# Optimization experiments

Hardware: AMD Instinct MI355X
Metric: run time of the kernel (lower is better)

The kernel has to match this reference:

```python
import jax, jax.numpy as jnp
import numpy as np

EPSILON = 0.01            # params.epsilon (cluster precision regularizer)
GAMMA = 0.005             # params.gamma (outlier/uniform component weight)
FIX_CLUSTER_POS_ITER = 1  # params.fix_cluster_pos_iter


def _sqdist(TVs, X):
    # TVs: (M, 3, N) transformed points, X: (K, 3) cluster means -> (M, N, K)
    return ((TVs ** 2).sum(1)[:, :, None]
            + (X ** 2).sum(1)[None, None, :]
            - 2.0 * jnp.einsum('mdn,kd->mnk', TVs, X))


def setup_inputs() -> dict:
    key = jax.random.key(0)
    kV, kX, kQ = jax.random.split(key, 3)
    M, N, K = 8, 8192, 256
    Vs = jax.random.normal(kV, (M, 3, N), dtype=jnp.float32)      # 3D point clouds
    X0 = jax.random.normal(kX, (K, 3), dtype=jnp.float32)         # init cluster means (sphere init)
    Q0 = 0.1 + 0.2 * jax.random.uniform(kQ, (K,), dtype=jnp.float32)  # init cluster precisions
    return {"Vs": Vs, "X0": X0, "Q0": Q0, "num_iters": 6}


def reference(Vs, X0, Q0, num_iters):
    M, _, N = Vs.shape
    K = X0.shape[0]
    dtype = Vs.dtype

    # mean_init: init_R = I, init_t = -mean(V) per view
    t0 = -Vs.mean(axis=2, keepdims=True)          # (M, 3, 1)
    TVs = Vs + t0
    beta = GAMMA * jnp.mean(Q0) ** 1.5            # get_default_beta(Q, gamma)

    X, Q = X0, Q0
    ds = _sqdist(TVs, X)                          # (M, N, K)
    R = jnp.broadcast_to(jnp.eye(3, dtype=dtype), (M, 3, 3))
    t = t0[:, :, 0]

    for i in range(num_iters):
        if i != num_iters - 1:  # detach everything except backprop_iter = [last]
            X = jax.lax.stop_gradient(X)
            Q = jax.lax.stop_gradient(Q)
            ds = jax.lax.stop_gradient(ds)

        # E-step: soft posteriors with uniform outlier component beta
        ap = jnp.exp(-0.5 * ds * Q) * Q ** 1.5    # (M, N, K); priors = 1, pyz_feature = 1
        a = ap / (ap.sum(axis=-1, keepdims=True) + beta)

        # M-step: weighted sufficient statistics
        L = a.sum(axis=1)                                   # (M, K)
        W = jnp.einsum('mdn,mnk->mdk', Vs, a) * Q           # (M, 3, K)
        mW = W.sum(axis=-1)                                 # (M, 3)
        b = L * Q                                           # (M, K)
        mX = jnp.einsum('mk,kd->md', b, X)                  # (M, 3)
        z = b.sum(axis=-1)                                  # (M,)

        # P = (W @ X)^T - mX mW^T / z  : 3x3 weighted cross-covariance per view
        P = (jnp.einsum('mdk,ke->med', W, X)
             - mX[:, :, None] * mW[:, None, :] / z[:, None, None])

        # batched Procrustes: R = U diag(1,1,det(U V^T)) V^T
        U, _, Vt = jnp.linalg.svd(P)
        det = jnp.linalg.det(jnp.einsum('mij,mjk->mik', U, Vt))
        sgn = jnp.concatenate([jnp.ones((M, 2), dtype), det[:, None]], axis=1)
        R = jnp.einsum('mij,mjk->mik', U * sgn[:, None, :], Vt)   # (M, 3, 3)
        t = (mX - jnp.einsum('mij,mj->mi', R, mW)) / z[:, None]   # (M, 3)
        TVs = jnp.einsum('mij,mjn->min', R, Vs) + t[:, :, None]   # (M, 3, N)

        # shared cluster updates (sum over views)
        den = L.sum(axis=0)                                 # (K,)
        if i > FIX_CLUSTER_POS_ITER:
            X = jnp.einsum('mdn,mnk->kd', TVs, a) / den[:, None]
        ds = _sqdist(TVs, X)
        wn = (a * ds).sum(axis=(0, 1))                      # (K,)
        Q = 3.0 * den / (wn + 3.0 * den * EPSILON)

    return TVs, R, t, X
```

## Files before the change

### kernel.cpp

```cpp
#include <hip/hip_runtime.h>
#include <math.h>

#define Mv 8
#define Nv 8192
#define Kv 256
#define BPM 64
#define NBLK (Mv*BPM)
#define NPB (Nv/BPM)
#define NITER 6
#define EPSILON_C 0.01f
#define GAMMA_C 0.005f

#define SWZK(k) ((((k)&63)<<2)|((k)>>6))
#define SWZP(p) ((((p)&31)<<2)|((p)>>5))

#define WS_R     0
#define WS_T     72
#define WS_X     96
#define WS_Q     864
#define WS_BETA  1120
#define WS_ACC   1124
#define AC_STATS 0
#define AC_L     128
#define AC_W     2176
#define AC_H     8320
#define ACCSZ    10368

__device__ __forceinline__ float wave_red_sum(float x) {
  int v;
  float t;
  v = __builtin_bit_cast(int, x);
  t = __builtin_bit_cast(float, __builtin_amdgcn_update_dpp(0, v, 0x111, 0xf, 0xf, true));
  x += t; v = __builtin_bit_cast(int, x);
  t = __builtin_bit_cast(float, __builtin_amdgcn_update_dpp(0, v, 0x112, 0xf, 0xf, true));
  x += t; v = __builtin_bit_cast(int, x);
  t = __builtin_bit_cast(float, __builtin_amdgcn_update_dpp(0, v, 0x114, 0xf, 0xf, true));
  x += t; v = __builtin_bit_cast(int, x);
  t = __builtin_bit_cast(float, __builtin_amdgcn_update_dpp(0, v, 0x118, 0xf, 0xf, true));
  x += t; v = __builtin_bit_cast(int, x);
  t = __builtin_bit_cast(float, __builtin_amdgcn_update_dpp(0, v, 0x142, 0xa, 0xf, false));
  x += t; v = __builtin_bit_cast(int, x);
  t = __builtin_bit_cast(float, __builtin_amdgcn_update_dpp(0, v, 0x143, 0xc, 0xf, false));
  x += t;
  return __builtin_bit_cast(float, __builtin_amdgcn_readlane(__builtin_bit_cast(int, x), 63));
}

__device__ __forceinline__ float quad_red_sum(float x) {
  int v = __builtin_bit_cast(int, x);
  float t = __builtin_bit_cast(float, __builtin_amdgcn_update_dpp(0, v, 0xB1, 0xf, 0xf, true));
  x += t; v = __builtin_bit_cast(int, x);
  t = __builtin_bit_cast(float, __builtin_amdgcn_update_dpp(0, v, 0x4E, 0xf, 0xf, true));
  x += t;
  return x;
}

__device__ __forceinline__ float sel4(int c, float a0, float a1, float a2, float a3) {
  float r = a0;
  r = (c==1) ? a1 : r;
  r = (c==2) ? a2 : r;
  r = (c==3) ? a3 : r;
  return r;
}

__global__ __launch_bounds__(256) void p0_init(const float* __restrict__ Vs,
                                               const float* __restrict__ X0,
                                               const float* __restrict__ Q0,
                                               float* __restrict__ ws) {
  __shared__ float sred[4];
  int tid = threadIdx.x;
  int b = blockIdx.x;
  int wave = tid >> 6, lane = tid & 63;
  if (b < 24) {
    int m = b / 3, d = b % 3;
    const float* src = Vs + (size_t)(m*3 + d) * Nv;
    float s = 0.f;
    for (int n = tid; n < Nv; n += 256) s += src[n];
    s = wave_red_sum(s);
    if (lane == 0) sred[wave] = s;
    __syncthreads();
    if (tid == 0) {
      float tot = sred[0]+sred[1]+sred[2]+sred[3];
      ws[WS_T + m*3 + d] = -tot / (float)Nv;
    }
    if (d == 0 && tid < 9) {
      ws[WS_R + m*9 + tid] = (tid==0||tid==4||tid==8) ? 1.f : 0.f;
    }
  } else {
    float s = (tid < Kv) ? Q0[tid] : 0.f;
    s = wave_red_sum(s);
    if (lane == 0) sred[wave] = s;
    __syncthreads();
    if (tid == 0) {
      float mq = (sred[0]+sred[1]+sred[2]+sred[3]) / (float)Kv;
      ws[WS_BETA] = GAMMA_C * mq * sqrtf(mq);
    }
    if (tid < Kv) ws[WS_Q + tid] = Q0[tid];
    for (int i = tid; i < Kv*3; i += 256) ws[WS_X + i] = X0[i];
    for (int i = tid; i < ACCSZ; i += 256) ws[WS_ACC + i] = 0.f;
  }
}

#define JROTF(app,aqq,apq,apr,aqr, vp0,vp1,vp2, vq0,vq1,vq2) do {           \
    float tau_ = (aqq - app) * __builtin_amdgcn_rcpf(2.0f*apq);             \
    float tt_ = __builtin_amdgcn_rcpf(fabsf(tau_) +                         \
                   __builtin_amdgcn_sqrtf(fmaf(tau_,tau_,1.0f)));           \
    tt_ = (tau_ < 0.0f) ? -tt_ : tt_;                                       \
    tt_ = (apq == 0.0f) ? 0.0f : tt_;                                       \
    float c_ = __builtin_amdgcn_rsqf(fmaf(tt_,tt_,1.0f)), s_ = tt_*c_;      \
    float papq_ = apq;                                                      \
    app = fmaf(-tt_,papq_,app); aqq = fmaf(tt_,papq_,aqq); apq = 0.0f;      \
    float tp_ = apr, tq_ = aqr;                                             \
    apr = c_*tp_ - s_*tq_; aqr = s_*tp_ + c_*tq_;                           \
    tp_=vp0; tq_=vq0; vp0=c_*tp_-s_*tq_; vq0=s_*tp_+c_*tq_;                 \
    tp_=vp1; tq_=vq1; vp1=c_*tp_-s_*tq_; vq1=s_*tp_+c_*tq_;                 \
    tp_=vp2; tq_=vq2; vp2=c_*tp_-s_*tq_; vq2=s_*tp_+c_*tq_;                 \
  } while(0)

#define CSWAP3F(la,lb, a0,a1,a2, b0,b1,b2) do {                             \
    if (la < lb) { float t_;                                                \
      t_=la; la=lb; lb=t_; t_=a0; a0=b0; b0=t_;                             \
      t_=a1; a1=b1; b1=t_; t_=a2; a2=b2; b2=t_; }                           \
  } while(0)

template<int ITPREV>
__device__ __forceinline__ void small_update(const float* __restrict__ acc,
                                             const float* __restrict__ ws,
                                             int tid,
                                             float (*sX)[3], float* sQ,
                                             float (*sR)[9], float (*sT)[3],
                                             float* sTn) {
  const int k = tid;
  float lk[Mv], w0v[Mv], w1v[Mv], w2v[Mv], hk[Mv];
  #pragma unroll
  for (int mm=0;mm<Mv;mm++) {
    lk[mm]  = acc[AC_L + mm*Kv + k];
    w0v[mm] = acc[AC_W + (mm*3+0)*Kv + k];
    w1v[mm] = acc[AC_W + (mm*3+1)*Kv + k];
    w2v[mm] = acc[AC_W + (mm*3+2)*Kv + k];
    hk[mm]  = acc[AC_H + mm*Kv + k];
  }
  float xp0 = 0.f, xp1 = 0.f, xp2 = 0.f;
  if (ITPREV <= 1) {
    xp0 = ws[WS_X + k*3+0]; xp1 = ws[WS_X + k*3+1]; xp2 = ws[WS_X + k*3+2];
  }

  if (tid < Mv) {
    int mm = tid;
    const float* st = acc + AC_STATS + mm*16;
    float s0=st[0], s1=st[1], s2v=st[2], s3=st[3], s4=st[4], s5=st[5],
          s6=st[6], s7=st[7], s8=st[8], s9=st[9], s10=st[10], s11=st[11],
          s12=st[12], s13=st[13], s14=st[14], s15=st[15];
    float z = s0;
    float mX0 = s1, mX1 = s2v, mX2 = s3;
    float mW0 = s4, mW1 = s5, mW2 = s6;
    float iz = __builtin_amdgcn_rcpf(z);
    float P00 = s7  - mX0*mW0*iz;
    float P01 = s8  - mX0*mW1*iz;
    float P02 = s9  - mX0*mW2*iz;
    float P10 = s10 - mX1*mW0*iz;
    float P11 = s11 - mX1*mW1*iz;
    float P12 = s12 - mX1*mW2*iz;
    float P20 = s13 - mX2*mW0*iz;
    float P21 = s14 - mX2*mW1*iz;
    float P22 = s15 - mX2*mW2*iz;
    float a00 = P00*P00 + P10*P10 + P20*P20;
    float a01 = P00*P01 + P10*P11 + P20*P21;
    float a02 = P00*P02 + P10*P12 + P20*P22;
    float a11 = P01*P01 + P11*P11 + P21*P21;
    float a12 = P01*P02 + P11*P12 + P21*P22;
    float a22 = P02*P02 + P12*P12 + P22*P22;
    float v00=1, v01=0, v02=0, v10=0, v11=1, v12=0, v20=0, v21=0, v22=1;
    #pragma unroll 1
    for (int sweep = 0; sweep < 8; sweep++) {
      JROTF(a00,a11,a01, a02,a12, v00,v10,v20, v01,v11,v21);
      JROTF(a00,a22,a02, a01,a12, v00,v10,v20, v02,v12,v22);
      JROTF(a11,a22,a12, a01,a02, v01,v11,v21, v02,v12,v22);
    }
    float l0 = a00, l1 = a11, l2 = a22;
    CSWAP3F(l0,l1, v00,v10,v20, v01,v11,v21);
    CSWAP3F(l1,l2, v01,v11,v21, v02,v12,v22);
    CSWAP3F(l0,l1, v00,v10,v20, v01,v11,v21);
    float detP = P00*(P11*P22-P12*P21) - P01*(P10*P22-P12*P20)
               + P02*(P10*P21-P11*P20);
    float s2d = (detP < 0.0f) ? -1.0f : 1.0f;
    float tiny = 1e-18f*l0 + 1e-30f;
    float w0i = __builtin_amdgcn_rsqf(fmaxf(l0,tiny));
    float w1i = __builtin_amdgcn_rsqf(fmaxf(l1,tiny));
    float w2i = s2d*__builtin_amdgcn_rsqf(fmaxf(l2,tiny));
    float M00 = w0i*v00*v00 + w1i*v01*v01 + w2i*v02*v02;
    float M01 = w0i*v00*v10 + w1i*v01*v11 + w2i*v02*v12;
    float M02 = w0i*v00*v20 + w1i*v01*v21 + w2i*v02*v22;
    float M11 = w0i*v10*v10 + w1i*v11*v11 + w2i*v12*v12;
    float M12 = w0i*v10*v20 + w1i*v11*v21 + w2i*v12*v22;
    float M22 = w0i*v20*v20 + w1i*v21*v21 + w2i*v22*v22;
    float R00n = P00*M00 + P01*M01 + P02*M02;
    float R01n = P00*M01 + P01*M11 + P02*M12;
    float R02n = P00*M02 + P01*M12 + P02*M22;
    float R10n = P10*M00 + P11*M01 + P12*M02;
    float R11n = P10*M01 + P11*M11 + P12*M12;
    float R12n = P10*M02 + P11*M12 + P12*M22;
    float R20n = P20*M00 + P21*M01 + P22*M02;
    float R21n = P20*M01 + P21*M11 + P22*M12;
    float R22n = P20*M02 + P21*M12 + P22*M22;
    float tm0 = (mX0 - (R00n*mW0 + R01n*mW1 + R02n*mW2))*iz;
    float tm1 = (mX1 - (R10n*mW0 + R11n*mW1 + R12n*mW2))*iz;
    float tm2 = (mX2 - (R20n*mW0 + R21n*mW1 + R22n*mW2))*iz;
    sR[mm][0]=R00n; sR[mm][1]=R01n; sR[mm][2]=R02n;
    sR[mm][3]=R10n; sR[mm][4]=R11n; sR[mm][5]=R12n;
    sR[mm][6]=R20n; sR[mm][7]=R21n; sR[mm][8]=R22n;
    sT[mm][0]=tm0; sT[mm][1]=tm1; sT[mm][2]=tm2;
    sTn[mm] = tm0*tm0 + tm1*tm1 + tm2*tm2;
  }
  __syncthreads();
  {
    float den = 0.f, Xn0=0.f, Xn1=0.f, Xn2=0.f, S2=0.f;
    #pragma unroll
    for (int mm=0;mm<Mv;mm++) {
      float r0 = sR[mm][0]*w0v[mm] + sR[mm][1]*w1v[mm] + sR[mm][2]*w2v[mm];
      float r1 = sR[mm][3]*w0v[mm] + sR[mm][4]*w1v[mm] + sR[mm][5]*w2v[mm];
      float r2 = sR[mm][6]*w0v[mm] + sR[mm][7]*w1v[mm] + sR[mm][8]*w2v[mm];
      float tt0 = sT[mm][0], tt1 = sT[mm][1], tt2 = sT[mm][2];
      den += lk[mm];
      Xn0 += r0 + tt0*lk[mm]; Xn1 += r1 + tt1*lk[mm]; Xn2 += r2 + tt2*lk[mm];
      S2  += hk[mm] + 2.f*(tt0*r0+tt1*r1+tt2*r2) + sTn[mm]*lk[mm];
    }
    float x0, x1, x2;
    if (ITPREV > 1) { float inv = __builtin_amdgcn_rcpf(den);
                      x0=Xn0*inv; x1=Xn1*inv; x2=Xn2*inv; }
    else            { x0=xp0; x1=xp1; x2=xp2; }
    float wn = S2 + (x0*x0+x1*x1+x2*x2)*den - 2.f*(x0*Xn0+x1*Xn1+x2*Xn2);
    float qn = 3.f*den / (wn + 3.f*den*EPSILON_C);
    sX[k][0]=x0; sX[k][1]=x1; sX[k][2]=x2;
    sQ[k] = qn;
  }
}

template<int IT>
__global__ __launch_bounds__(256) void p_iter(const float* __restrict__ Vs,
                                              float* __restrict__ ws) {
  __shared__ __align__(16) float sC4[Kv][4];
  __shared__ float sKC[Kv];
  __shared__ __align__(16) float sP4[NPB][4];
  __shared__ __align__(16) float sV4[NPB][4];
  __shared__ float sLi[NPB];
  __shared__ float st4[4][16];
  __shared__ float sX[Kv][3];
  __shared__ float sQ[Kv];
  __shared__ float sR[Mv][9];
  __shared__ float sT[Mv][3];
  __shared__ float sTn[Mv];

  int tid  = threadIdx.x;
  int wave = tid >> 6, lane = tid & 63;
  int bid  = blockIdx.x;
  int m    = bid / BPM;
  int blk  = bid % BPM;
  int n0   = blk * NPB;

  float* acc  = ws + WS_ACC + (IT % 3)*ACCSZ;
  float* accz = ws + WS_ACC + ((IT+1) % 3)*ACCSZ;
  float beta = ws[WS_BETA];

  if (IT == 0) {
    if (tid < 72) ((float*)sR)[tid] = ws[WS_R + tid];
    if (tid < 24) ((float*)sT)[tid] = ws[WS_T + tid];
    sX[tid][0] = ws[WS_X + 3*tid+0];
    sX[tid][1] = ws[WS_X + 3*tid+1];
    sX[tid][2] = ws[WS_X + 3*tid+2];
    sQ[tid]    = ws[WS_Q + tid];
  } else {
    const float* accp = ws + WS_ACC + ((IT+2) % 3)*ACCSZ;
    small_update<(IT > 0) ? (IT-1) : 0>(accp, ws, tid, sX, sQ, sR, sT, sTn);
  }
  __syncthreads();

  { int base = bid*21;
    if (tid < 21 && base + tid < ACCSZ) accz[base + tid] = 0.f; }

  const float L2E = 1.4426950408889634f;
  {
    float xx = sX[tid][0], xy = sX[tid][1], xz = sX[tid][2];
    float q  = sQ[tid];
    float qL = q * L2E;
    float kA = -0.5f*qL;
    float kB = kA*(xx*xx+xy*xy+xz*xz);
    float kQ32 = q*sqrtf(q);
    int rr = SWZK(tid);
    *reinterpret_cast<float4*>(&sC4[rr][0]) = make_float4(qL*xx, qL*xy, qL*xz, kA);
    sKC[rr] = kQ32 * __builtin_amdgcn_exp2f(kB);
  }
  if (tid < NPB) {
    float R00=sR[m][0],R01=sR[m][1],R02=sR[m][2];
    float R10=sR[m][3],R11=sR[m][4],R12=sR[m][5];
    float R20=sR[m][6],R21=sR[m][7],R22=sR[m][8];
    float t0=sT[m][0], t1=sT[m][1], t2=sT[m][2];
    int n = n0 + tid;
    float vx = Vs[(size_t)(m*3+0)*Nv + n];
    float vy = Vs[(size_t)(m*3+1)*Nv + n];
    float vz = Vs[(size_t)(m*3+2)*Nv + n];
    float px = fmaf(R00,vx, fmaf(R01,vy, fmaf(R02,vz, t0)));
    float py = fmaf(R10,vx, fmaf(R11,vy, fmaf(R12,vz, t1)));
    float pz = fmaf(R20,vx, fmaf(R21,vy, fmaf(R22,vz, t2)));
    float tvn = fmaf(px,px, fmaf(py,py, pz*pz));
    float vn  = fmaf(vx,vx, fmaf(vy,vy, vz*vz));
    int pr = SWZP(tid);
    *reinterpret_cast<float4*>(&sP4[pr][0]) = make_float4(px,py,pz,tvn);
    *reinterpret_cast<float4*>(&sV4[pr][0]) = make_float4(vx,vy,vz,vn);
  }
  __syncthreads();

  {
    int ks = tid & 3, pg = tid >> 2;
    float4 P0 = *reinterpret_cast<const float4*>(&sP4[SWZP(2*pg+0)][0]);
    float4 P1 = *reinterpret_cast<const float4*>(&sP4[SWZP(2*pg+1)][0]);
    float s0 = 0.f, s1 = 0.f;
    #pragma unroll 4
    for (int j = 0; j < Kv/4; j++) {
      int row = (j<<2) | ks;
      float4 c4 = *reinterpret_cast<const float4*>(&sC4[row][0]);
      float kc = sKC[row];
      float a0 = fmaf(P0.x,c4.x, fmaf(P0.y,c4.y, fmaf(P0.z,c4.z, P0.w*c4.w)));
      float a1 = fmaf(P1.x,c4.x, fmaf(P1.y,c4.y, fmaf(P1.z,c4.z, P1.w*c4.w)));
      s0 = fmaf(__builtin_amdgcn_exp2f(a0), kc, s0);
      s1 = fmaf(__builtin_amdgcn_exp2f(a1), kc, s1);
    }
    float S0 = quad_red_sum(s0);
    float S1 = quad_red_sum(s1);
    if (ks < 2) {
      float Ssel = (ks == 1) ? S1 : S0;
      sLi[SWZP(2*pg + ks)] = -__log2f(Ssel + beta);
    }
  }
  __syncthreads();

  float cXx0,cXy0,cXz0,cA0,cC0, cXx1,cXy1,cXz1,cA1,cC1,
        cXx2,cXy2,cXz2,cA2,cC2, cXx3,cXy3,cXz3,cA3,cC3;
  {
    int kg = tid >> 2;
    #define LDC(c) { int rr = SWZK(4*kg + c); \
      float4 t4 = *reinterpret_cast<const float4*>(&sC4[rr][0]); \
      cXx##c=t4.x; cXy##c=t4.y; cXz##c=t4.z; cA##c=t4.w; cC##c=sKC[rr]; }
    LDC(0) LDC(1) LDC(2) LDC(3)
    #undef LDC
  }
  float L0=0,L1=0,L2=0,L3=0, Wx0=0,Wx1=0,Wx2=0,Wx3=0,
        Wy0=0,Wy1=0,Wy2=0,Wy3=0, Wz0=0,Wz1=0,Wz2=0,Wz3=0,
        H0=0,H1=0,H2=0,H3=0;
  {
    int ns = tid & 3;
    #pragma unroll 4
    for (int j = 0; j < NPB/4; j++) {
      int prow = (j<<2) | ns;
      float4 p4 = *reinterpret_cast<const float4*>(&sP4[prow][0]);
      float4 v4 = *reinterpret_cast<const float4*>(&sV4[prow][0]);
      float li = sLi[prow];
      #define P2K(c) { \
        float arg = fmaf(p4.w, cA##c, li); \
        arg = fmaf(p4.x, cXx##c, fmaf(p4.y, cXy##c, fmaf(p4.z, cXz##c, arg))); \
        float e = __builtin_amdgcn_exp2f(arg) * cC##c; \
        L##c += e; \
        Wx##c = fmaf(e, v4.x, Wx##c); Wy##c = fmaf(e, v4.y, Wy##c); \
        Wz##c = fmaf(e, v4.z, Wz##c); H##c  = fmaf(e, v4.w, H##c); }
      P2K(0) P2K(1) P2K(2) P2K(3)
      #undef P2K
    }
  }
  L0=quad_red_sum(L0); L1=quad_red_sum(L1); L2=quad_red_sum(L2); L3=quad_red_sum(L3);
  Wx0=quad_red_sum(Wx0); Wx1=quad_red_sum(Wx1); Wx2=quad_red_sum(Wx2); Wx3=quad_red_sum(Wx3);
  Wy0=quad_red_sum(Wy0); Wy1=quad_red_sum(Wy1); Wy2=quad_red_sum(Wy2); Wy3=quad_red_sum(Wy3);
  Wz0=quad_red_sum(Wz0); Wz1=quad_red_sum(Wz1); Wz2=quad_red_sum(Wz2); Wz3=quad_red_sum(Wz3);
  H0=quad_red_sum(H0); H1=quad_red_sum(H1); H2=quad_red_sum(H2); H3=quad_red_sum(H3);
  int c = tid & 3;
  float vL  = sel4(c, L0,L1,L2,L3);
  float vWx = sel4(c, Wx0,Wx1,Wx2,Wx3);
  float vWy = sel4(c, Wy0,Wy1,Wy2,Wy3);
  float vWz = sel4(c, Wz0,Wz1,Wz2,Wz3);
  float vH  = sel4(c, H0,H1,H2,H3);
  atomicAdd(&acc[AC_L + m*Kv + tid], vL);
  atomicAdd(&acc[AC_W + (m*3+0)*Kv + tid], vWx);
  atomicAdd(&acc[AC_W + (m*3+1)*Kv + tid], vWy);
  atomicAdd(&acc[AC_W + (m*3+2)*Kv + tid], vWz);
  atomicAdd(&acc[AC_H + m*Kv + tid], vH);

  {
    float q  = sQ[tid];
    float x0 = sX[tid][0], x1 = sX[tid][1], x2 = sX[tid][2];
    float bk = vL*q;
    float sw0 = vWx*q, sw1 = vWy*q, sw2 = vWz*q;
    float pr[16];
    pr[0]=bk;  pr[1]=bk*x0; pr[2]=bk*x1; pr[3]=bk*x2;
    pr[4]=sw0; pr[5]=sw1;   pr[6]=sw2;
    pr[7]=sw0*x0;  pr[8]=sw1*x0;  pr[9]=sw2*x0;
    pr[10]=sw0*x1; pr[11]=sw1*x1; pr[12]=sw2*x1;
    pr[13]=sw0*x2; pr[14]=sw1*x2; pr[15]=sw2*x2;
    float red[16];
    #pragma unroll
    for (int v2=0; v2<16; v2++) red[v2] = wave_red_sum(pr[v2]);
    if (lane == 0) {
      #pragma unroll
      for (int v2=0; v2<16; v2++) st4[wave][v2] = red[v2];
    }
    __syncthreads();
    if (tid < 16)
      atomicAdd(&acc[AC_STATS + m*16 + ((tid + blk) & 15)],
                st4[0][(tid+blk)&15]+st4[1][(tid+blk)&15]+
                st4[2][(tid+blk)&15]+st4[3][(tid+blk)&15]);
  }
}

#define OUT_TOTAL (Mv*3*Nv + 72 + 24 + Kv*3)
__global__ __launch_bounds__(256) void p3_final(const float* __restrict__ Vs,
                                                const float* __restrict__ ws,
                                                float* __restrict__ out) {
  __shared__ float sX[Kv][3];
  __shared__ float sQ[Kv];
  __shared__ float sR[Mv][9];
  __shared__ float sT[Mv][3];
  __shared__ float sTn[Mv];
  int tid = threadIdx.x;
  const float* acc = ws + WS_ACC + ((NITER-1) % 3)*ACCSZ;
  small_update<NITER-1>(acc, ws, tid, sX, sQ, sR, sT, sTn);
  __syncthreads();

  for (int idx = blockIdx.x*256 + tid; idx < OUT_TOTAL; idx += 256*256) {
    if (idx < Mv*3*Nv) {
      int m = idx / (3*Nv);
      int r = idx % (3*Nv);
      int d = r / Nv;
      int n = r % Nv;
      float vx = Vs[(size_t)(m*3+0)*Nv + n];
      float vy = Vs[(size_t)(m*3+1)*Nv + n];
      float vz = Vs[(size_t)(m*3+2)*Nv + n];
      out[idx] = fmaf(sR[m][d*3+0],vx,
                 fmaf(sR[m][d*3+1],vy,
                 fmaf(sR[m][d*3+2],vz, sT[m][d])));
    } else {
      int j = idx - Mv*3*Nv;
      float v;
      if (j < 72)      v = ((float*)sR)[j];
      else if (j < 96) v = ((float*)sT)[j-72];
      else             v = ((float*)sX)[j-96];
      out[idx] = v;
    }
  }
}

extern "C" void kernel_launch(void* const* d_in, const int* in_sizes, int n_in,
                              void* d_out, int out_size, void* d_ws, size_t ws_size,
                              hipStream_t stream) {
  const float* Vs = (const float*)d_in[0];
  const float* X0 = (const float*)d_in[1];
  const float* Q0 = (const float*)d_in[2];
  float* out = (float*)d_out;
  float* ws  = (float*)d_ws;

  p0_init<<<25, 256, 0, stream>>>(Vs, X0, Q0, ws);
  p_iter<0><<<NBLK, 256, 0, stream>>>(Vs, ws);
  p_iter<1><<<NBLK, 256, 0, stream>>>(Vs, ws);
  p_iter<2><<<NBLK, 256, 0, stream>>>(Vs, ws);
  p_iter<3><<<NBLK, 256, 0, stream>>>(Vs, ws);
  p_iter<4><<<NBLK, 256, 0, stream>>>(Vs, ws);
  p_iter<5><<<NBLK, 256, 0, stream>>>(Vs, ws);
  p3_final<<<256, 256, 0, stream>>>(Vs, ws, out);
}
```

Measured before the change: 183.6 us.

## Fuse all iterations into one persistent kernel with grid-wide barriers

Replaces the init kernel, six per-iteration launches and the final kernel with a single persistent kernel that loops over iterations and uses an atomic counter barrier between them. Each block keeps its slice of points in shared memory across iterations and computes the view mean and beta itself, which removes launch gaps and repeated global reloads of Vs. Final outputs are written from shared data per block. It relies on all 512 blocks being co-resident, or the barrier deadlocks. The memset only zeroes the barrier and the first accumulator buffer, so correctness depends on the in-kernel zeroing of the other rotating buffers.

```diff
diff --git a/kernel.cpp b/kernel.cpp
--- a/kernel.cpp
+++ b/kernel.cpp
@@ -6,6 +6,7 @@
 #define Kv 256
 #define BPM 64
 #define NBLK (Mv*BPM)
+#define NBLK_U 512u
 #define NPB (Nv/BPM)
 #define NITER 6
 #define EPSILON_C 0.01f
@@ -14,17 +15,26 @@
 #define SWZK(k) ((((k)&63)<<2)|((k)>>6))
 #define SWZP(p) ((((p)&31)<<2)|((p)>>5))
 
-#define WS_R     0
-#define WS_T     72
-#define WS_X     96
-#define WS_Q     864
-#define WS_BETA  1120
-#define WS_ACC   1124
+#define WS_BAR   0
+#define WS_ACC   16
 #define AC_STATS 0
 #define AC_L     128
 #define AC_W     2176
 #define AC_H     8320
 #define ACCSZ    10368
+
+__device__ __forceinline__ void gsync(unsigned* bar, int tid) {
+  __threadfence();
+  __syncthreads();
+  if (tid == 0) {
+    __hip_atomic_fetch_add(bar, 1u, __ATOMIC_RELEASE, __HIP_MEMORY_SCOPE_AGENT);
+    while (__hip_atomic_load(bar, __ATOMIC_ACQUIRE, __HIP_MEMORY_SCOPE_AGENT) < NBLK_U) {
+      __builtin_amdgcn_s_sleep(2);
+    }
+  }
+  __syncthreads();
+  __threadfence();
+}
 
 __device__ __forceinline__ float wave_red_sum(float x) {
   int v;
@@ -60,44 +70,6 @@
   r = (c==2) ? a2 : r;
   r = (c==3) ? a3 : r;
   return r;
-}
-
-__global__ __launch_bounds__(256) void p0_init(const float* __restrict__ Vs,
-                                               const float* __restrict__ X0,
-                                               const float* __restrict__ Q0,
-                                               float* __restrict__ ws) {
-  __shared__ float sred[4];
-  int tid = threadIdx.x;
-  int b = blockIdx.x;
-  int wave = tid >> 6, lane = tid & 63;
-  if (b < 24) {
-    int m = b / 3, d = b % 3;
-    const float* src = Vs + (size_t)(m*3 + d) * Nv;
-    float s = 0.f;
-    for (int n = tid; n < Nv; n += 256) s += src[n];
-    s = wave_red_sum(s);
-    if (lane == 0) sred[wave] = s;
-    __syncthreads();
-    if (tid == 0) {
-      float tot = sred[0]+sred[1]+sred[2]+sred[3];
-      ws[WS_T + m*3 + d] = -tot / (float)Nv;
-    }
-    if (d == 0 && tid < 9) {
-      ws[WS_R + m*9 + tid] = (tid==0||tid==4||tid==8) ? 1.f : 0.f;
-    }
-  } else {
-    float s = (tid < Kv) ? Q0[tid] : 0.f;
-    s = wave_red_sum(s);
-    if (lane == 0) sred[wave] = s;
-    __syncthreads();
-    if (tid == 0) {
-      float mq = (sred[0]+sred[1]+sred[2]+sred[3]) / (float)Kv;
-      ws[WS_BETA] = GAMMA_C * mq * sqrtf(mq);
-    }
-    if (tid < Kv) ws[WS_Q + tid] = Q0[tid];
-    for (int i = tid; i < Kv*3; i += 256) ws[WS_X + i] = X0[i];
-    for (int i = tid; i < ACCSZ; i += 256) ws[WS_ACC + i] = 0.f;
-  }
 }
 
 #define JROTF(app,aqq,apq,apr,aqr, vp0,vp1,vp2, vq0,vq1,vq2) do {           \
@@ -122,13 +94,12 @@
       t_=a1; a1=b1; b1=t_; t_=a2; a2=b2; b2=t_; }                           \
   } while(0)
 
-template<int ITPREV>
-__device__ __forceinline__ void small_update(const float* __restrict__ acc,
-                                             const float* __restrict__ ws,
-                                             int tid,
-                                             float (*sX)[3], float* sQ,
-                                             float (*sR)[9], float (*sT)[3],
-                                             float* sTn) {
+__device__ __forceinline__ void small_update_rt(const float* __restrict__ acc,
+                                                const float* __restrict__ X0,
+                                                bool useX0, int tid,
+                                                float (*sX)[3], float* sQ,
+                                                float (*sR)[9], float (*sT)[3],
+                                                float* sTn) {
   const int k = tid;
   float lk[Mv], w0v[Mv], w1v[Mv], w2v[Mv], hk[Mv];
   #pragma unroll
@@ -140,8 +111,8 @@
     hk[mm]  = acc[AC_H + mm*Kv + k];
   }
   float xp0 = 0.f, xp1 = 0.f, xp2 = 0.f;
-  if (ITPREV <= 1) {
-    xp0 = ws[WS_X + k*3+0]; xp1 = ws[WS_X + k*3+1]; xp2 = ws[WS_X + k*3+2];
+  if (useX0) {
+    xp0 = X0[k*3+0]; xp1 = X0[k*3+1]; xp2 = X0[k*3+2];
   }
 
   if (tid < Mv) {
@@ -225,9 +196,9 @@
       S2  += hk[mm] + 2.f*(tt0*r0+tt1*r1+tt2*r2) + sTn[mm]*lk[mm];
     }
     float x0, x1, x2;
-    if (ITPREV > 1) { float inv = __builtin_amdgcn_rcpf(den);
-                      x0=Xn0*inv; x1=Xn1*inv; x2=Xn2*inv; }
-    else            { x0=xp0; x1=xp1; x2=xp2; }
+    if (!useX0) { float inv = __builtin_amdgcn_rcpf(den);
+                  x0=Xn0*inv; x1=Xn1*inv; x2=Xn2*inv; }
+    else        { x0=xp0; x1=xp1; x2=xp2; }
     float wn = S2 + (x0*x0+x1*x1+x2*x2)*den - 2.f*(x0*Xn0+x1*Xn1+x2*Xn2);
     float qn = 3.f*den / (wn + 3.f*den*EPSILON_C);
     sX[k][0]=x0; sX[k][1]=x1; sX[k][2]=x2;
@@ -235,9 +206,12 @@
   }
 }
 
-template<int IT>
-__global__ __launch_bounds__(256) void p_iter(const float* __restrict__ Vs,
-                                              float* __restrict__ ws) {
+#define OUT_TVS (Mv*3*Nv)
+__global__ __launch_bounds__(256, 2) void fused(const float* __restrict__ Vs,
+                                                const float* __restrict__ X0,
+                                                const float* __restrict__ Q0,
+                                                float* __restrict__ ws,
+                                                float* __restrict__ out) {
   __shared__ __align__(16) float sC4[Kv][4];
   __shared__ float sKC[Kv];
   __shared__ __align__(16) float sP4[NPB][4];
@@ -249,6 +223,8 @@
   __shared__ float sR[Mv][9];
   __shared__ float sT[Mv][3];
   __shared__ float sTn[Mv];
+  __shared__ float sredq[4];
+  __shared__ float sredt[12];
 
   int tid  = threadIdx.x;
   int wave = tid >> 6, lane = tid & 63;
@@ -257,190 +233,208 @@
   int blk  = bid % BPM;
   int n0   = blk * NPB;
 
-  float* acc  = ws + WS_ACC + (IT % 3)*ACCSZ;
-  float* accz = ws + WS_ACC + ((IT+1) % 3)*ACCSZ;
-  float beta = ws[WS_BETA];
-
-  if (IT == 0) {
-    if (tid < 72) ((float*)sR)[tid] = ws[WS_R + tid];
-    if (tid < 24) ((float*)sT)[tid] = ws[WS_T + tid];
-    sX[tid][0] = ws[WS_X + 3*tid+0];
-    sX[tid][1] = ws[WS_X + 3*tid+1];
-    sX[tid][2] = ws[WS_X + 3*tid+2];
-    sQ[tid]    = ws[WS_Q + tid];
-  } else {
-    const float* accp = ws + WS_ACC + ((IT+2) % 3)*ACCSZ;
-    small_update<(IT > 0) ? (IT-1) : 0>(accp, ws, tid, sX, sQ, sR, sT, sTn);
-  }
+  unsigned* bar = reinterpret_cast<unsigned*>(ws) + WS_BAR;
+  float* accs = ws + WS_ACC;
+
+  float q_own = Q0[tid];
+  { float s = wave_red_sum(q_own);
+    if (lane == 0) sredq[wave] = s; }
+
+  const float* V0 = Vs + (size_t)(m*3+0)*Nv;
+  const float* V1 = Vs + (size_t)(m*3+1)*Nv;
+  const float* V2 = Vs + (size_t)(m*3+2)*Nv;
+  { float sx=0.f, sy=0.f, sz=0.f;
+    for (int n = tid; n < Nv; n += 256) { sx += V0[n]; sy += V1[n]; sz += V2[n]; }
+    sx = wave_red_sum(sx); sy = wave_red_sum(sy); sz = wave_red_sum(sz);
+    if (lane == 0) { sredt[wave] = sx; sredt[4+wave] = sy; sredt[8+wave] = sz; } }
   __syncthreads();
-
-  { int base = bid*21;
-    if (tid < 21 && base + tid < ACCSZ) accz[base + tid] = 0.f; }
+  float beta;
+  { float mq = (sredq[0]+sredq[1]+sredq[2]+sredq[3]) * (1.f/(float)Kv);
+    beta = GAMMA_C * mq * sqrtf(mq); }
+  float t00 = -(sredt[0]+sredt[1]+sredt[2]+sredt[3]) * (1.f/(float)Nv);
+  float t01 = -(sredt[4]+sredt[5]+sredt[6]+sredt[7]) * (1.f/(float)Nv);
+  float t02 = -(sredt[8]+sredt[9]+sredt[10]+sredt[11]) * (1.f/(float)Nv);
+
+  float vx=0.f, vy=0.f, vz=0.f, vn=0.f;
+  if (tid < NPB) {
+    int n = n0 + tid;
+    vx = V0[n]; vy = V1[n]; vz = V2[n];
+    vn = fmaf(vx,vx, fmaf(vy,vy, vz*vz));
+    *reinterpret_cast<float4*>(&sV4[SWZP(tid)][0]) = make_float4(vx,vy,vz,vn);
+  }
 
   const float L2E = 1.4426950408889634f;
-  {
-    float xx = sX[tid][0], xy = sX[tid][1], xz = sX[tid][2];
-    float q  = sQ[tid];
-    float qL = q * L2E;
-    float kA = -0.5f*qL;
-    float kB = kA*(xx*xx+xy*xy+xz*xz);
-    float kQ32 = q*sqrtf(q);
-    int rr = SWZK(tid);
-    *reinterpret_cast<float4*>(&sC4[rr][0]) = make_float4(qL*xx, qL*xy, qL*xz, kA);
-    sKC[rr] = kQ32 * __builtin_amdgcn_exp2f(kB);
-  }
-  if (tid < NPB) {
-    float R00=sR[m][0],R01=sR[m][1],R02=sR[m][2];
-    float R10=sR[m][3],R11=sR[m][4],R12=sR[m][5];
-    float R20=sR[m][6],R21=sR[m][7],R22=sR[m][8];
-    float t0=sT[m][0], t1=sT[m][1], t2=sT[m][2];
-    int n = n0 + tid;
-    float vx = Vs[(size_t)(m*3+0)*Nv + n];
-    float vy = Vs[(size_t)(m*3+1)*Nv + n];
-    float vz = Vs[(size_t)(m*3+2)*Nv + n];
-    float px = fmaf(R00,vx, fmaf(R01,vy, fmaf(R02,vz, t0)));
-    float py = fmaf(R10,vx, fmaf(R11,vy, fmaf(R12,vz, t1)));
-    float pz = fmaf(R20,vx, fmaf(R21,vy, fmaf(R22,vz, t2)));
-    float tvn = fmaf(px,px, fmaf(py,py, pz*pz));
-    float vn  = fmaf(vx,vx, fmaf(vy,vy, vz*vz));
-    int pr = SWZP(tid);
-    *reinterpret_cast<float4*>(&sP4[pr][0]) = make_float4(px,py,pz,tvn);
-    *reinterpret_cast<float4*>(&sV4[pr][0]) = make_float4(vx,vy,vz,vn);
-  }
+  #pragma unroll 1
+  for (int it = 0; it < NITER; ++it) {
+    float* acc  = accs + (it % 3)*ACCSZ;
+    float* accz = accs + ((it+1) % 3)*ACCSZ;
+
+    if (it == 0) {
+      sX[tid][0] = X0[3*tid+0];
+      sX[tid][1] = X0[3*tid+1];
+      sX[tid][2] = X0[3*tid+2];
+      sQ[tid]    = q_own;
+    } else {
+      const float* accp = accs + ((it+2) % 3)*ACCSZ;
+      small_update_rt(accp, X0, (it-1) <= 1, tid, sX, sQ, sR, sT, sTn);
+    }
+    __syncthreads();
+
+    if (it < NITER-1) {
+      int base = bid*21;
+      if (tid < 21 && base + tid < ACCSZ) accz[base + tid] = 0.f;
+    }
+
+    float R00,R01,R02,R10,R11,R12,R20,R21,R22, t0,t1,t2;
+    if (it == 0) {
+      R00=1;R01=0;R02=0; R10=0;R11=1;R12=0; R20=0;R21=0;R22=1;
+      t0=t00; t1=t01; t2=t02;
+    } else {
+      R00=sR[m][0];R01=sR[m][1];R02=sR[m][2];
+      R10=sR[m][3];R11=sR[m][4];R12=sR[m][5];
+      R20=sR[m][6];R21=sR[m][7];R22=sR[m][8];
+      t0=sT[m][0]; t1=sT[m][1]; t2=sT[m][2];
+    }
+
+    {
+      float xx = sX[tid][0], xy = sX[tid][1], xz = sX[tid][2];
+      float q  = sQ[tid];
+      float qL = q * L2E;
+      float kA = -0.5f*qL;
+      float kB = kA*(xx*xx+xy*xy+xz*xz);
+      float kQ32 = q*sqrtf(q);
+      int rr = SWZK(tid);
+      *reinterpret_cast<float4*>(&sC4[rr][0]) = make_float4(qL*xx, qL*xy, qL*xz, kA);
+      sKC[rr] = kQ32 * __builtin_amdgcn_exp2f(kB);
+    }
+    if (tid < NPB) {
+      float px = fmaf(R00,vx, fmaf(R01,vy, fmaf(R02,vz, t0)));
+      float py = fmaf(R10,vx, fmaf(R11,vy, fmaf(R12,vz, t1)));
+      float pz = fmaf(R20,vx, fmaf(R21,vy, fmaf(R22,vz, t2)));
+      float tvn = fmaf(px,px, fmaf(py,py, pz*pz));
+      *reinterpret_cast<float4*>(&sP4[SWZP(tid)][0]) = make_float4(px,py,pz,tvn);
+    }
+    __syncthreads();
+
+    {
+      int ks = tid & 3, pg = tid >> 2;
+      float4 P0 = *reinterpret_cast<const float4*>(&sP4[SWZP(2*pg+0)][0]);
+      float4 P1 = *reinterpret_cast<const float4*>(&sP4[SWZP(2*pg+1)][0]);
+      float s0 = 0.f, s1 = 0.f;
+      #pragma unroll 4
+      for (int j = 0; j < Kv/4; j++) {
+        int row = (j<<2) | ks;
+        float4 c4 = *reinterpret_cast<const float4*>(&sC4[row][0]);
+        float kc = sKC[row];
+        float a0 = fmaf(P0.x,c4.x, fmaf(P0.y,c4.y, fmaf(P0.z,c4.z, P0.w*c4.w)));
+        float a1 = fmaf(P1.x,c4.x, fmaf(P1.y,c4.y, fmaf(P1.z,c4.z, P1.w*c4.w)));
+        s0 = fmaf(__builtin_amdgcn_exp2f(a0), kc, s0);
+        s1 = fmaf(__builtin_amdgcn_exp2f(a1), kc, s1);
+      }
+      float S0 = quad_red_sum(s0);
+      float S1 = quad_red_sum(s1);
+      if (ks < 2) {
+        float Ssel = (ks == 1) ? S1 : S0;
+        sLi[SWZP(2*pg + ks)] = -__log2f(Ssel + beta);
+      }
+    }
+    __syncthreads();
+
+    float cXx0,cXy0,cXz0,cA0,cC0, cXx1,cXy1,cXz1,cA1,cC1,
+          cXx2,cXy2,cXz2,cA2,cC2, cXx3,cXy3,cXz3,cA3,cC3;
+    {
+      int kg = tid >> 2;
+      #define LDC(c) { int rr = SWZK(4*kg + c); \
+        float4 t4 = *reinterpret_cast<const float4*>(&sC4[rr][0]); \
+        cXx##c=t4.x; cXy##c=t4.y; cXz##c=t4.z; cA##c=t4.w; cC##c=sKC[rr]; }
+      LDC(0) LDC(1) LDC(2) LDC(3)
+      #undef LDC
+    }
+    float L0=0,L1=0,L2=0,L3=0, Wx0=0,Wx1=0,Wx2=0,Wx3=0,
+          Wy0=0,Wy1=0,Wy2=0,Wy3=0, Wz0=0,Wz1=0,Wz2=0,Wz3=0,
+          H0=0,H1=0,H2=0,H3=0;
+    {
+      int ns = tid & 3;
+      #pragma unroll 4
+      for (int j = 0; j < NPB/4; j++) {
+        int prow = (j<<2) | ns;
+        float4 p4 = *reinterpret_cast<const float4*>(&sP4[prow][0]);
+        float4 v4 = *reinterpret_cast<const float4*>(&sV4[prow][0]);
+        float li = sLi[prow];
+        #define P2K(c) { \
+          float arg = fmaf(p4.w, cA##c, li); \
+          arg = fmaf(p4.x, cXx##c, fmaf(p4.y, cXy##c, fmaf(p4.z, cXz##c, arg))); \
+          float e = __builtin_amdgcn_exp2f(arg) * cC##c; \
+          L##c += e; \
+          Wx##c = fmaf(e, v4.x, Wx##c); Wy##c = fmaf(e, v4.y, Wy##c); \
+          Wz##c = fmaf(e, v4.z, Wz##c); H##c  = fmaf(e, v4.w, H##c); }
+        P2K(0) P2K(1) P2K(2) P2K(3)
+        #undef P2K
+      }
+    }
+    L0=quad_red_sum(L0); L1=quad_red_sum(L1); L2=quad_red_sum(L2); L3=quad_red_sum(L3);
+    Wx0=quad_red_sum(Wx0); Wx1=quad_red_sum(Wx1); Wx2=quad_red_sum(Wx2); Wx3=quad_red_sum(Wx3);
+    Wy0=quad_red_sum(Wy0); Wy1=quad_red_sum(Wy1); Wy2=quad_red_sum(Wy2); Wy3=quad_red_sum(Wy3);
+    Wz0=quad_red_sum(Wz0); Wz1=quad_red_sum(Wz1); Wz2=quad_red_sum(Wz2); Wz3=quad_red_sum(Wz3);
+    H0=quad_red_sum(H0); H1=quad_red_sum(H1); H2=quad_red_sum(H2); H3=quad_red_sum(H3);
+    int c = tid & 3;
+    float vL  = sel4(c, L0,L1,L2,L3);
+    float vWx = sel4(c, Wx0,Wx1,Wx2,Wx3);
+    float vWy = sel4(c, Wy0,Wy1,Wy2,Wy3);
+    float vWz = sel4(c, Wz0,Wz1,Wz2,Wz3);
+    float vH  = sel4(c, H0,H1,H2,H3);
+    atomicAdd(&acc[AC_L + m*Kv + tid], vL);
+    atomicAdd(&acc[AC_W + (m*3+0)*Kv + tid], vWx);
+    atomicAdd(&acc[AC_W + (m*3+1)*Kv + tid], vWy);
+    atomicAdd(&acc[AC_W + (m*3+2)*Kv + tid], vWz);
+    atomicAdd(&acc[AC_H + m*Kv + tid], vH);
+
+    {
+      float q  = sQ[tid];
+      float x0 = sX[tid][0], x1 = sX[tid][1], x2 = sX[tid][2];
+      float bk = vL*q;
+      float sw0 = vWx*q, sw1 = vWy*q, sw2 = vWz*q;
+      float pr[16];
+      pr[0]=bk;  pr[1]=bk*x0; pr[2]=bk*x1; pr[3]=bk*x2;
+      pr[4]=sw0; pr[5]=sw1;   pr[6]=sw2;
+      pr[7]=sw0*x0;  pr[8]=sw1*x0;  pr[9]=sw2*x0;
+      pr[10]=sw0*x1; pr[11]=sw1*x1; pr[12]=sw2*x1;
+      pr[13]=sw0*x2; pr[14]=sw1*x2; pr[15]=sw2*x2;
+      float red[16];
+      #pragma unroll
+      for (int v2=0; v2<16; v2++) red[v2] = wave_red_sum(pr[v2]);
+      if (lane == 0) {
+        #pragma unroll
+        for (int v2=0; v2<16; v2++) st4[wave][v2] = red[v2];
+      }
+      __syncthreads();
+      if (tid < 16)
+        atomicAdd(&acc[AC_STATS + m*16 + ((tid + blk) & 15)],
+                  st4[0][(tid+blk)&15]+st4[1][(tid+blk)&15]+
+                  st4[2][(tid+blk)&15]+st4[3][(tid+blk)&15]);
+    }
+
+    gsync(bar + it, tid);
+  }
+
+  small_update_rt(accs + ((NITER-1) % 3)*ACCSZ, X0, false, tid, sX, sQ, sR, sT, sTn);
   __syncthreads();
 
-  {
-    int ks = tid & 3, pg = tid >> 2;
-    float4 P0 = *reinterpret_cast<const float4*>(&sP4[SWZP(2*pg+0)][0]);
-    float4 P1 = *reinterpret_cast<const float4*>(&sP4[SWZP(2*pg+1)][0]);
-    float s0 = 0.f, s1 = 0.f;
-    #pragma unroll 4
-    for (int j = 0; j < Kv/4; j++) {
-      int row = (j<<2) | ks;
-      float4 c4 = *reinterpret_cast<const float4*>(&sC4[row][0]);
-      float kc = sKC[row];
-      float a0 = fmaf(P0.x,c4.x, fmaf(P0.y,c4.y, fmaf(P0.z,c4.z, P0.w*c4.w)));
-      float a1 = fmaf(P1.x,c4.x, fmaf(P1.y,c4.y, fmaf(P1.z,c4.z, P1.w*c4.w)));
-      s0 = fmaf(__builtin_amdgcn_exp2f(a0), kc, s0);
-      s1 = fmaf(__builtin_amdgcn_exp2f(a1), kc, s1);
-    }
-    float S0 = quad_red_sum(s0);
-    float S1 = quad_red_sum(s1);
-    if (ks < 2) {
-      float Ssel = (ks == 1) ? S1 : S0;
-      sLi[SWZP(2*pg + ks)] = -__log2f(Ssel + beta);
-    }
-  }
-  __syncthreads();
-
-  float cXx0,cXy0,cXz0,cA0,cC0, cXx1,cXy1,cXz1,cA1,cC1,
-        cXx2,cXy2,cXz2,cA2,cC2, cXx3,cXy3,cXz3,cA3,cC3;
-  {
-    int kg = tid >> 2;
-    #define LDC(c) { int rr = SWZK(4*kg + c); \
-      float4 t4 = *reinterpret_cast<const float4*>(&sC4[rr][0]); \
-      cXx##c=t4.x; cXy##c=t4.y; cXz##c=t4.z; cA##c=t4.w; cC##c=sKC[rr]; }
-    LDC(0) LDC(1) LDC(2) LDC(3)
-    #undef LDC
-  }
-  float L0=0,L1=0,L2=0,L3=0, Wx0=0,Wx1=0,Wx2=0,Wx3=0,
-        Wy0=0,Wy1=0,Wy2=0,Wy3=0, Wz0=0,Wz1=0,Wz2=0,Wz3=0,
-        H0=0,H1=0,H2=0,H3=0;
-  {
-    int ns = tid & 3;
-    #pragma unroll 4
-    for (int j = 0; j < NPB/4; j++) {
-      int prow = (j<<2) | ns;
-      float4 p4 = *reinterpret_cast<const float4*>(&sP4[prow][0]);
-      float4 v4 = *reinterpret_cast<const float4*>(&sV4[prow][0]);
-      float li = sLi[prow];
-      #define P2K(c) { \
-        float arg = fmaf(p4.w, cA##c, li); \
-        arg = fmaf(p4.x, cXx##c, fmaf(p4.y, cXy##c, fmaf(p4.z, cXz##c, arg))); \
-        float e = __builtin_amdgcn_exp2f(arg) * cC##c; \
-        L##c += e; \
-        Wx##c = fmaf(e, v4.x, Wx##c); Wy##c = fmaf(e, v4.y, Wy##c); \
-        Wz##c = fmaf(e, v4.z, Wz##c); H##c  = fmaf(e, v4.w, H##c); }
-      P2K(0) P2K(1) P2K(2) P2K(3)
-      #undef P2K
-    }
-  }
-  L0=quad_red_sum(L0); L1=quad_red_sum(L1); L2=quad_red_sum(L2); L3=quad_red_sum(L3);
-  Wx0=quad_red_sum(Wx0); Wx1=quad_red_sum(Wx1); Wx2=quad_red_sum(Wx2); Wx3=quad_red_sum(Wx3);
-  Wy0=quad_red_sum(Wy0); Wy1=quad_red_sum(Wy1); Wy2=quad_red_sum(Wy2); Wy3=quad_red_sum(Wy3);
-  Wz0=quad_red_sum(Wz0); Wz1=quad_red_sum(Wz1); Wz2=quad_red_sum(Wz2); Wz3=quad_red_sum(Wz3);
-  H0=quad_red_sum(H0); H1=quad_red_sum(H1); H2=quad_red_sum(H2); H3=quad_red_sum(H3);
-  int c = tid & 3;
-  float vL  = sel4(c, L0,L1,L2,L3);
-  float vWx = sel4(c, Wx0,Wx1,Wx2,Wx3);
-  float vWy = sel4(c, Wy0,Wy1,Wy2,Wy3);
-  float vWz = sel4(c, Wz0,Wz1,Wz2,Wz3);
-  float vH  = sel4(c, H0,H1,H2,H3);
-  atomicAdd(&acc[AC_L + m*Kv + tid], vL);
-  atomicAdd(&acc[AC_W + (m*3+0)*Kv + tid], vWx);
-  atomicAdd(&acc[AC_W + (m*3+1)*Kv + tid], vWy);
-  atomicAdd(&acc[AC_W + (m*3+2)*Kv + tid], vWz);
-  atomicAdd(&acc[AC_H + m*Kv + tid], vH);
-
-  {
-    float q  = sQ[tid];
-    float x0 = sX[tid][0], x1 = sX[tid][1], x2 = sX[tid][2];
-    float bk = vL*q;
-    float sw0 = vWx*q, sw1 = vWy*q, sw2 = vWz*q;
-    float pr[16];
-    pr[0]=bk;  pr[1]=bk*x0; pr[2]=bk*x1; pr[3]=bk*x2;
-    pr[4]=sw0; pr[5]=sw1;   pr[6]=sw2;
-    pr[7]=sw0*x0;  pr[8]=sw1*x0;  pr[9]=sw2*x0;
-    pr[10]=sw0*x1; pr[11]=sw1*x1; pr[12]=sw2*x1;
-    pr[13]=sw0*x2; pr[14]=sw1*x2; pr[15]=sw2*x2;
-    float red[16];
-    #pragma unroll
-    for (int v2=0; v2<16; v2++) red[v2] = wave_red_sum(pr[v2]);
-    if (lane == 0) {
-      #pragma unroll
-      for (int v2=0; v2<16; v2++) st4[wave][v2] = red[v2];
-    }
-    __syncthreads();
-    if (tid < 16)
-      atomicAdd(&acc[AC_STATS + m*16 + ((tid + blk) & 15)],
-                st4[0][(tid+blk)&15]+st4[1][(tid+blk)&15]+
-                st4[2][(tid+blk)&15]+st4[3][(tid+blk)&15]);
-  }
-}
-
-#define OUT_TOTAL (Mv*3*Nv + 72 + 24 + Kv*3)
-__global__ __launch_bounds__(256) void p3_final(const float* __restrict__ Vs,
-                                                const float* __restrict__ ws,
-                                                float* __restrict__ out) {
-  __shared__ float sX[Kv][3];
-  __shared__ float sQ[Kv];
-  __shared__ float sR[Mv][9];
-  __shared__ float sT[Mv][3];
-  __shared__ float sTn[Mv];
-  int tid = threadIdx.x;
-  const float* acc = ws + WS_ACC + ((NITER-1) % 3)*ACCSZ;
-  small_update<NITER-1>(acc, ws, tid, sX, sQ, sR, sT, sTn);
-  __syncthreads();
-
-  for (int idx = blockIdx.x*256 + tid; idx < OUT_TOTAL; idx += 256*256) {
-    if (idx < Mv*3*Nv) {
-      int m = idx / (3*Nv);
-      int r = idx % (3*Nv);
-      int d = r / Nv;
-      int n = r % Nv;
-      float vx = Vs[(size_t)(m*3+0)*Nv + n];
-      float vy = Vs[(size_t)(m*3+1)*Nv + n];
-      float vz = Vs[(size_t)(m*3+2)*Nv + n];
-      out[idx] = fmaf(sR[m][d*3+0],vx,
-                 fmaf(sR[m][d*3+1],vy,
-                 fmaf(sR[m][d*3+2],vz, sT[m][d])));
-    } else {
-      int j = idx - Mv*3*Nv;
+  for (int i = tid; i < 3*NPB; i += 256) {
+    int d  = i >> 7;
+    int nn = i & (NPB-1);
+    float4 v4 = *reinterpret_cast<const float4*>(&sV4[SWZP(nn)][0]);
+    out[(size_t)(m*3+d)*Nv + n0 + nn] =
+      fmaf(sR[m][d*3+0], v4.x, fmaf(sR[m][d*3+1], v4.y,
+      fmaf(sR[m][d*3+2], v4.z, sT[m][d])));
+  }
+  if (bid == 0) {
+    for (int j = tid; j < 72 + 24 + Kv*3; j += 256) {
       float v;
       if (j < 72)      v = ((float*)sR)[j];
       else if (j < 96) v = ((float*)sT)[j-72];
       else             v = ((float*)sX)[j-96];
-      out[idx] = v;
+      out[(size_t)OUT_TVS + j] = v;
     }
   }
 }
@@ -454,12 +448,6 @@
   float* out = (float*)d_out;
   float* ws  = (float*)d_ws;
 
-  p0_init<<<25, 256, 0, stream>>>(Vs, X0, Q0, ws);
-  p_iter<0><<<NBLK, 256, 0, stream>>>(Vs, ws);
-  p_iter<1><<<NBLK, 256, 0, stream>>>(Vs, ws);
-  p_iter<2><<<NBLK, 256, 0, stream>>>(Vs, ws);
-  p_iter<3><<<NBLK, 256, 0, stream>>>(Vs, ws);
-  p_iter<4><<<NBLK, 256, 0, stream>>>(Vs, ws);
-  p_iter<5><<<NBLK, 256, 0, stream>>>(Vs, ws);
-  p3_final<<<256, 256, 0, stream>>>(Vs, ws, out);
-}
+  hipMemsetAsync(ws, 0, (WS_ACC + ACCSZ) * sizeof(float), stream);
+  fused<<<NBLK, 256, 0, stream>>>(Vs, X0, Q0, ws, out);
+}
```

Result: slower. 682.1 us (+271.6%).
